# Performance work log

Measured on AMD Instinct MI355X. Metric: run time of the kernel, lower is better.

## Reference

```python
import jax, jax.numpy as jnp
import numpy as np

N = 100000       # num nodes
E = 1600000      # num edges (before self loops)
IN = 128         # in_channels
H = 4            # heads (layer 1)
C = 64           # hidden_channels
BN_EPS = 1e-5
NEG_SLOPE = 0.2  # PyG GATConv default


def setup_inputs() -> dict:
    key = jax.random.key(0)
    ks = jax.random.split(key, 12)
    s = lambda k, shape: jax.random.normal(k, shape, jnp.float32) * 0.05
    return {
        "x": jax.random.normal(ks[0], (N, IN), jnp.float32),
        "edge_index": jax.random.randint(ks[1], (2, E), 0, N),
        # GATConv layer 1: in=128 -> 64 per head, 4 heads, concat
        "W1": s(ks[2], (IN, H * C)),
        "a_src1": s(ks[3], (H, C)),
        "a_dst1": s(ks[4], (H, C)),
        "b1": jnp.zeros((H * C,), jnp.float32),
        # BatchNorm1d(256), eval mode with default running stats
        "bn_gamma": jnp.ones((H * C,), jnp.float32),
        "bn_beta": jnp.zeros((H * C,), jnp.float32),
        # GATConv layer 2: 256 -> 1, heads=1, concat=False
        "W2": s(ks[5], (H * C, 1)),
        "a_src2": s(ks[6], (1, 1)),
        "a_dst2": s(ks[7], (1, 1)),
        "b2": jnp.zeros((1,), jnp.float32),
        # risk predictor MLP: Linear(1,64) -> ReLU -> Linear(64,1) -> Sigmoid
        "mlp_w1": s(ks[8], (1, C)),
        "mlp_b1": jnp.zeros((C,), jnp.float32),
        "mlp_w2": s(ks[9], (C, 1)),
        "mlp_b2": jnp.zeros((1,), jnp.float32),
    }


def gat_conv(x, W, a_s, a_d, b, src, dst, n, concat):
    """PyG-style GATConv (self loops already appended to src/dst)."""
    h_, c_ = a_s.shape
    h = (x @ W).reshape(n, h_, c_)                       # [N,H,C]
    alpha_src = jnp.einsum('nhc,hc->nh', h, a_s)          # [N,H]
    alpha_dst = jnp.einsum('nhc,hc->nh', h, a_d)          # [N,H]
    alpha = jax.nn.leaky_relu(alpha_src[src] + alpha_dst[dst], NEG_SLOPE)  # [E,H]
    # segment softmax over destination nodes (self loops guarantee nonempty segments)
    amax = jax.ops.segment_max(alpha, dst, num_segments=n)
    ex = jnp.exp(alpha - amax[dst])
    den = jax.ops.segment_sum(ex, dst, num_segments=n)
    coef = ex / den[dst]                                  # [E,H]
    out = jax.ops.segment_sum(h[src] * coef[..., None], dst, num_segments=n)  # [N,H,C]
    out = out.reshape(n, h_ * c_) if concat else out.mean(axis=1)
    return out + b


def reference(x, edge_index, W1, a_src1, a_dst1, b1, bn_gamma, bn_beta,
              W2, a_src2, a_dst2, b2, mlp_w1, mlp_b1, mlp_w2, mlp_b2):
    n = x.shape[0]
    loops = jnp.arange(n)
    src = jnp.concatenate([edge_index[0], loops])
    dst = jnp.concatenate([edge_index[1], loops])

    h = gat_conv(x, W1, a_src1, a_dst1, b1, src, dst, n, concat=True)   # [N,256]
    # BatchNorm1d eval: running_mean=0, running_var=1
    h = h / jnp.sqrt(jnp.float32(1.0 + BN_EPS)) * bn_gamma + bn_beta
    h = jax.nn.elu(h)
    # dropout is identity in eval mode
    h = gat_conv(h, W2, a_src2, a_dst2, b2, src, dst, n, concat=False)  # [N,1]

    risk = jax.nn.relu(h @ mlp_w1 + mlp_b1)
    risk = jax.nn.sigmoid(risk @ mlp_w2 + mlp_b2)                        # [N,1]
    return risk
```

## Files before the change

kernel.cpp:

```cpp
#include <hip/hip_runtime.h>
#include <math.h>

#define NSL 0.2f
#define BSH 8
#define CAP 4608
#define ECHUNK 4096
#define MAXNB 512

typedef __attribute__((ext_vector_type(8))) short bf16x8;
typedef __attribute__((ext_vector_type(4))) float f32x4;
typedef __attribute__((ext_vector_type(2))) float floatx2;

__device__ __forceinline__ unsigned short f2b(float f){
  unsigned int u = __builtin_bit_cast(unsigned int, f);
  u = (u + 0x7FFFu + ((u >> 16) & 1u)) >> 16;
  return (unsigned short)u;
}
__device__ __forceinline__ unsigned cvtpk_bf16(float a, float b){
  unsigned r; asm("v_cvt_pk_bf16_f32 %0, %1, %2" : "=v"(r) : "v"(a), "v"(b)); return r;
}
__device__ __forceinline__ void pkfma(floatx2& a, floatx2 x, floatx2 w){
  asm("v_pk_fma_f32 %0, %1, %2, %0" : "+v"(a) : "v"(x), "v"(w));
}

__global__ __launch_bounds__(256) void k_fused1(const float* __restrict__ W, unsigned short* __restrict__ wt,
                                                const int* __restrict__ esrc, const int* __restrict__ edst,
                                                int E, int NB, int* gCur, unsigned* __restrict__ ebuf,
                                                int prepBlocks){
  __shared__ int hist[MAXNB];
  __shared__ int base[MAXNB];
  int bid = blockIdx.x, t = threadIdx.x;
  if (bid < prepBlocks){
    int idx = bid*256 + t;
    int k = idx >> 8, ch = idx & 255;
    wt[ch*128 + k] = f2b(W[idx]);
    return;
  }
  int b0 = bid - prepBlocks;
  for (int i=t;i<NB;i+=256) hist[i] = 0;
  __syncthreads();
  int e0 = b0*ECHUNK;
  int srcv[16], dstv[16];
  #pragma unroll
  for (int j=0;j<16;j++){
    int e = e0 + t + j*256;
    if (e < E){ srcv[j] = esrc[e]; dstv[j] = edst[e]; atomicAdd(&hist[dstv[j]>>BSH], 1); }
    else dstv[j] = -1;
  }
  __syncthreads();
  for (int i=t;i<NB;i+=256){
    int h = hist[i];
    base[i] = h > 0 ? atomicAdd(&gCur[i], h) : 0;
    hist[i] = 0;
  }
  __syncthreads();
  #pragma unroll
  for (int j=0;j<16;j++){
    if (dstv[j] >= 0){
      int b = dstv[j]>>BSH;
      int pos = base[b] + atomicAdd(&hist[b], 1);
      if (pos < CAP)
        ebuf[(size_t)b*CAP + pos] = (unsigned)srcv[j] | ((unsigned)(dstv[j] & 255) << 17);
    }
  }
}

__global__ __launch_bounds__(256) void k_fused2(const unsigned short* __restrict__ w1t,
                                                const float* __restrict__ x,
                                                const float* __restrict__ a_s1,
                                                const float* __restrict__ a_d1,
                                                unsigned char* __restrict__ h1f8,
                                                float* __restrict__ asrc, float* __restrict__ adst,
                                                int N, int gemmBlocks,
                                                const int* __restrict__ gCur, const unsigned* __restrict__ ebuf,
                                                int* __restrict__ rows, int* __restrict__ deg,
                                                int* __restrict__ csr){
  __shared__ union SM {
    unsigned short xs[64][132];
    struct { int lcnt[256]; int rofs[256]; int csr_l[CAP+256]; } c;
  } sm;
  int tid = threadIdx.x;
  int bid = blockIdx.x;

  if (bid < gemmBlocks){
    int lane = tid & 63, w = tid >> 6;
    int g = lane >> 4, nr = lane & 15;
    int n0 = bid*64;
    #pragma unroll
    for (int i=0;i<8;i++){
      int idx = tid + i*256;
      int node = idx >> 5, c4 = idx & 31;
      int gn = n0 + node;
      float4 v = (gn < N) ? *(const float4*)&x[(size_t)gn*128 + c4*4] : make_float4(0,0,0,0);
      uint2 pk = { cvtpk_bf16(v.x, v.y), cvtpk_bf16(v.z, v.w) };
      *(uint2*)&sm.xs[node][c4*4] = pk;
    }
    __syncthreads();

    int node_f[4]; bool val_f[4];
    #pragma unroll
    for (int fn=0;fn<4;fn++){ node_f[fn] = n0 + fn*16 + nr; val_f[fn] = node_f[fn] < N; }

    f32x4 acc[4][4] = {};
    #pragma unroll
    for (int s=0;s<4;s++){
      int ks = s*32;
      bf16x8 af[4], bf[4];
      #pragma unroll
      for (int fm=0;fm<4;fm++){
        int ch = w*64 + fm*16 + nr;
        const ushort4 lo = *(const ushort4*)(w1t + ch*128 + ks + 4*g);
        const ushort4 hi = *(const ushort4*)(w1t + ch*128 + ks + 16 + 4*g);
        af[fm] = (bf16x8){ (short)lo.x,(short)lo.y,(short)lo.z,(short)lo.w,
                           (short)hi.x,(short)hi.y,(short)hi.z,(short)hi.w };
      }
      #pragma unroll
      for (int fn=0;fn<4;fn++){
        union { uint2 u2[2]; bf16x8 v; } bb;
        bb.u2[0] = *(const uint2*)&sm.xs[fn*16 + nr][ks + 4*g];
        bb.u2[1] = *(const uint2*)&sm.xs[fn*16 + nr][ks + 16 + 4*g];
        bf[fn] = bb.v;
      }
      #pragma unroll
      for (int fm=0;fm<4;fm++)
        #pragma unroll
        for (int fn=0;fn<4;fn++)
          acc[fm][fn] = __builtin_amdgcn_mfma_f32_16x16x32_bf16(af[fm], bf[fn], acc[fm][fn], 0, 0, 0);
    }

    float ps[4] = {0.f,0.f,0.f,0.f}, pd[4] = {0.f,0.f,0.f,0.f};
    #pragma unroll
    for (int fm=0;fm<4;fm++){
      int cb = w*64 + fm*16 + g*4;
      float4 av = *(const float4*)&a_s1[cb];
      float4 dv = *(const float4*)&a_d1[cb];
      #pragma unroll
      for (int fn=0;fn<4;fn++){
        f32x4 c = acc[fm][fn];
        if (val_f[fn]){
          int u = __builtin_amdgcn_cvt_pk_fp8_f32(c[0], c[1], 0, false);
          u = __builtin_amdgcn_cvt_pk_fp8_f32(c[2], c[3], u, true);
          *(unsigned int*)(h1f8 + (size_t)node_f[fn]*256 + cb) = (unsigned int)u;
        }
        ps[fn] += c[0]*av.x + c[1]*av.y + c[2]*av.z + c[3]*av.w;
        pd[fn] += c[0]*dv.x + c[1]*dv.y + c[2]*dv.z + c[3]*dv.w;
      }
    }
    #pragma unroll
    for (int fn=0;fn<4;fn++){
      ps[fn] += __shfl_xor(ps[fn], 16); ps[fn] += __shfl_xor(ps[fn], 32);
      pd[fn] += __shfl_xor(pd[fn], 16); pd[fn] += __shfl_xor(pd[fn], 32);
      if (g == 0 && val_f[fn]){
        asrc[node_f[fn]*4 + w] = ps[fn];
        adst[node_f[fn]*4 + w] = pd[fn];
      }
    }
  } else {
    int b = bid - gemmBlocks;
    int node0 = b<<BSH;
    int nNodes = min(256, N - node0);
    int cnt_b = min(gCur[b], CAP);
    sm.c.lcnt[tid] = 0;
    __syncthreads();
    const unsigned* eb = ebuf + (size_t)b*CAP;
    for (int i=tid;i<cnt_b;i+=256) atomicAdd(&sm.c.lcnt[eb[i]>>17], 1);
    __syncthreads();
    int v = (tid < nNodes) ? (sm.c.lcnt[tid] + 1) : 0;
    sm.c.rofs[tid] = v; __syncthreads();
    #pragma unroll
    for (int o=1;o<256;o<<=1){
      int xv = (tid>=o) ? sm.c.rofs[tid-o] : 0; __syncthreads();
      sm.c.rofs[tid] += xv; __syncthreads();
    }
    int excl = sm.c.rofs[tid] - v;
    if (tid < nNodes) sm.c.csr_l[excl] = node0 + tid;
    sm.c.lcnt[tid] = excl + 1;
    __syncthreads();
    for (int i=tid;i<cnt_b;i+=256){
      unsigned e = eb[i];
      int pos = atomicAdd(&sm.c.lcnt[e>>17], 1);
      sm.c.csr_l[pos] = (int)(e & 0x1FFFFu);
    }
    __syncthreads();
    int total = sm.c.rofs[255];
    int gbase = b*(CAP+256);
    for (int i=tid;i<total;i+=256) csr[gbase+i] = sm.c.csr_l[i];
    if (tid < nNodes){ rows[node0+tid] = gbase + excl; deg[node0+tid] = v; }
  }
}

__global__ __launch_bounds__(256) void k_agg1(const int* __restrict__ rows, const int* __restrict__ deg,
                                              const int* __restrict__ csr,
                                              const unsigned char* __restrict__ h1f8,
                                              const float* __restrict__ asrc, const float* __restrict__ adst,
                                              const float* __restrict__ b1,
                                              const float* __restrict__ gamma, const float* __restrict__ beta,
                                              const float* __restrict__ W2,
                                              float* __restrict__ h2, int N){
  int lane = threadIdx.x & 63, wv = threadIdx.x >> 6;
  int node = blockIdx.x*4 + wv;
  if (node >= N) return;
  int slot = lane >> 4, l4 = lane & 15;
  int head = l4 >> 2;
  int rs = rows[node], d = deg[node];
  float adh = adst[node*4 + head];
  const uint4* h1u4 = (const uint4*)h1f8;
  floatx2 acc2[8];
  #pragma unroll
  for (int j=0;j<8;j++){ acc2[j][0] = 0.f; acc2[j][1] = 0.f; }
  float den = 0.f;
  int i = slot;
  if (i < d){
    int s = csr[rs+i];
    float aa = asrc[s*4 + head];
    uint4 v = h1u4[(size_t)s*16 + l4];
    while (true){
      int in = i + 4;
      bool hn = in < d;
      int sn = hn ? csr[rs+in] : 0;
      float al = aa + adh;
      al = fmaxf(al, NSL*al);
      float wgt = __expf(al);
      den += wgt;
      floatx2 ww; ww[0] = wgt; ww[1] = wgt;
      floatx2 f;
      f = __builtin_amdgcn_cvt_pk_f32_fp8(v.x, false); pkfma(acc2[0], f, ww);
      f = __builtin_amdgcn_cvt_pk_f32_fp8(v.x, true ); pkfma(acc2[1], f, ww);
      f = __builtin_amdgcn_cvt_pk_f32_fp8(v.y, false); pkfma(acc2[2], f, ww);
      f = __builtin_amdgcn_cvt_pk_f32_fp8(v.y, true ); pkfma(acc2[3], f, ww);
      f = __builtin_amdgcn_cvt_pk_f32_fp8(v.z, false); pkfma(acc2[4], f, ww);
      f = __builtin_amdgcn_cvt_pk_f32_fp8(v.z, true ); pkfma(acc2[5], f, ww);
      f = __builtin_amdgcn_cvt_pk_f32_fp8(v.w, false); pkfma(acc2[6], f, ww);
      f = __builtin_amdgcn_cvt_pk_f32_fp8(v.w, true ); pkfma(acc2[7], f, ww);
      if (!hn) break;
      i = in;
      aa = asrc[sn*4 + head];
      v = h1u4[(size_t)sn*16 + l4];
    }
  }
  #pragma unroll
  for (int j=0;j<8;j++){
    acc2[j][0] += __shfl_xor(acc2[j][0],16); acc2[j][1] += __shfl_xor(acc2[j][1],16);
    acc2[j][0] += __shfl_xor(acc2[j][0],32); acc2[j][1] += __shfl_xor(acc2[j][1],32);
  }
  den += __shfl_xor(den,16); den += __shfl_xor(den,32);
  float inv = 1.f/den;
  const float bsc = 0.99999500003749968f;
  int c = l4*16;
  float p = 0.f;
  #pragma unroll
  for (int q=0;q<4;q++){
    int cq = c + q*4;
    float4 bb = *(const float4*)&b1[cq];
    float4 gg = *(const float4*)&gamma[cq];
    float4 be = *(const float4*)&beta[cq];
    float4 w2_ = *(const float4*)&W2[cq];
    float o0 = (acc2[q*2+0][0]*inv + bb.x)*bsc*gg.x + be.x;
    float o1 = (acc2[q*2+0][1]*inv + bb.y)*bsc*gg.y + be.y;
    float o2 = (acc2[q*2+1][0]*inv + bb.z)*bsc*gg.z + be.z;
    float o3 = (acc2[q*2+1][1]*inv + bb.w)*bsc*gg.w + be.w;
    o0 = (o0>0.f)?o0:(__expf(o0)-1.f); o1 = (o1>0.f)?o1:(__expf(o1)-1.f);
    o2 = (o2>0.f)?o2:(__expf(o2)-1.f); o3 = (o3>0.f)?o3:(__expf(o3)-1.f);
    p += o0*w2_.x + o1*w2_.y + o2*w2_.z + o3*w2_.w;
  }
  p += __shfl_xor(p,1); p += __shfl_xor(p,2); p += __shfl_xor(p,4); p += __shfl_xor(p,8);
  if (lane == 0) h2[node] = p;
}

__global__ __launch_bounds__(256) void k_agg2(const int* __restrict__ rows, const int* __restrict__ deg,
                       const int* __restrict__ csr, const float* __restrict__ h2,
                       const float* __restrict__ as2, const float* __restrict__ ad2,
                       const float* __restrict__ b2,
                       const float* __restrict__ mw1, const float* __restrict__ mb1,
                       const float* __restrict__ mw2, const float* __restrict__ mb2,
                       float* __restrict__ out, int N){
  int t = threadIdx.x;
  int g16 = t >> 4, l = t & 15;
  int n = blockIdx.x*16 + g16;
  if (n >= N) return;
  float a_s = as2[0], a_d = ad2[0];
  float hd = h2[n];
  float ad = hd * a_d;
  int rs = rows[n], d = deg[n];
  float den = 0.f, num = 0.f;
  for (int i=l;i<d;i+=16){
    int s = csr[rs+i];
    float hs = h2[s];
    float al = hs*a_s + ad;
    al = fmaxf(al, NSL*al);
    float w = __expf(al);
    den += w; num += w*hs;
  }
  #pragma unroll
  for (int o=1;o<16;o<<=1){ den += __shfl_xor(den,o); num += __shfl_xor(num,o); }
  float o2 = num/den + b2[0];
  float acc = 0.f;
  #pragma unroll
  for (int q=0;q<4;q++){
    int j = l + q*16;
    float r = fmaxf(o2*mw1[j] + mb1[j], 0.f);
    acc += r*mw2[j];
  }
  #pragma unroll
  for (int o=1;o<16;o<<=1) acc += __shfl_xor(acc,o);
  if (l == 0) out[n] = 1.f/(1.f + __expf(-(acc + mb2[0])));
}

extern "C" void kernel_launch(void* const* d_in, const int* in_sizes, int n_in,
                              void* d_out, int out_size, void* d_ws, size_t ws_size,
                              hipStream_t stream){
  const float* x   = (const float*)d_in[0];
  const int*   ei  = (const int*)  d_in[1];
  const float* W1  = (const float*)d_in[2];
  const float* as1 = (const float*)d_in[3];
  const float* ad1 = (const float*)d_in[4];
  const float* b1  = (const float*)d_in[5];
  const float* gam = (const float*)d_in[6];
  const float* bet = (const float*)d_in[7];
  const float* W2  = (const float*)d_in[8];
  const float* as2 = (const float*)d_in[9];
  const float* ad2 = (const float*)d_in[10];
  const float* b2  = (const float*)d_in[11];
  const float* mw1 = (const float*)d_in[12];
  const float* mb1 = (const float*)d_in[13];
  const float* mw2 = (const float*)d_in[14];
  const float* mb2 = (const float*)d_in[15];
  float* out = (float*)d_out;

  int N = in_sizes[0] / 128;
  int E = in_sizes[1] / 2;
  const int* esrc = ei;
  const int* edst = ei + E;
  int NB = (N + 255) >> 8;

  char* p = (char*)d_ws;
  auto alloc = [&](size_t bytes)->char*{ char* r = p; p += (bytes + 255) & ~(size_t)255; return r; };
  int*      deg   = (int*)     alloc((size_t)N*4);
  int*      rows  = (int*)     alloc((size_t)N*4);
  int*      gCur  = (int*)     alloc((size_t)NB*4);
  unsigned* ebuf  = (unsigned*)alloc((size_t)NB*CAP*4);
  int*      csr   = (int*)     alloc((size_t)NB*(CAP+256)*4);
  unsigned short* w1t  = (unsigned short*)alloc((size_t)256*128*2);
  unsigned char*  h1f8 = (unsigned char*) alloc((size_t)N*256);
  float* asrc  = (float*)alloc((size_t)N*4*4);
  float* adst  = (float*)alloc((size_t)N*4*4);
  float* h2    = (float*)alloc((size_t)N*4);

  hipMemsetAsync(gCur, 0, (size_t)NB*4, stream);

  int prepBlocks = 128;
  int nbA = (E + ECHUNK - 1)/ECHUNK;
  k_fused1<<<prepBlocks + nbA, 256, 0, stream>>>(W1, w1t, esrc, edst, E, NB, gCur, ebuf, prepBlocks);

  int gemmBlocks = (N + 63)/64;
  k_fused2<<<gemmBlocks + NB, 256, 0, stream>>>(w1t, x, as1, ad1, h1f8, asrc, adst,
                                                N, gemmBlocks, gCur, ebuf, rows, deg, csr);

  k_agg1<<<(N+3)/4,256,0,stream>>>(rows, deg, csr, h1f8, asrc, adst, b1, gam, bet, W2, h2, N);

  k_agg2<<<(N+15)/16,256,0,stream>>>(rows, deg, csr, h2, as2, ad2, b2, mw1, mb1, mw2, mb2, out, N);
}
```

Baseline: 217.3 us.

## Quantize layer-1 features to FP4 with per-node-per-head scales

```diff
diff --git a/kernel.cpp b/kernel.cpp
--- a/kernel.cpp
+++ b/kernel.cpp
@@ -6,6 +6,21 @@
 #define CAP 4608
 #define ECHUNK 4096
 #define MAXNB 512
+
+#if defined(__has_builtin)
+#if __has_builtin(__builtin_amdgcn_cvt_scalef32_pk_f32_fp4) && __has_builtin(__builtin_amdgcn_cvt_scalef32_pk_fp4_f32)
+#define HAS_FP4 1
+#endif
+#endif
+#ifndef HAS_FP4
+#define HAS_FP4 0
+#endif
+
+#if HAS_FP4
+#define ROWB 128
+#else
+#define ROWB 256
+#endif
 
 typedef __attribute__((ext_vector_type(8))) short bf16x8;
 typedef __attribute__((ext_vector_type(4))) float f32x4;
@@ -69,8 +84,8 @@
                                                 const float* __restrict__ x,
                                                 const float* __restrict__ a_s1,
                                                 const float* __restrict__ a_d1,
-                                                unsigned char* __restrict__ h1f8,
-                                                float* __restrict__ asrc, float* __restrict__ adst,
+                                                unsigned char* __restrict__ h1q,
+                                                float2* __restrict__ asz, float* __restrict__ adst,
                                                 int N, int gemmBlocks,
                                                 const int* __restrict__ gCur, const unsigned* __restrict__ ebuf,
                                                 int* __restrict__ rows, int* __restrict__ deg,
@@ -128,7 +143,7 @@
           acc[fm][fn] = __builtin_amdgcn_mfma_f32_16x16x32_bf16(af[fm], bf[fn], acc[fm][fn], 0, 0, 0);
     }
 
-    float ps[4] = {0.f,0.f,0.f,0.f}, pd[4] = {0.f,0.f,0.f,0.f};
+    float ps[4] = {0.f,0.f,0.f,0.f}, pd[4] = {0.f,0.f,0.f,0.f}, qm[4] = {0.f,0.f,0.f,0.f};
     #pragma unroll
     for (int fm=0;fm<4;fm++){
       int cb = w*64 + fm*16 + g*4;
@@ -137,21 +152,51 @@
       #pragma unroll
       for (int fn=0;fn<4;fn++){
         f32x4 c = acc[fm][fn];
-        if (val_f[fn]){
-          int u = __builtin_amdgcn_cvt_pk_fp8_f32(c[0], c[1], 0, false);
-          u = __builtin_amdgcn_cvt_pk_fp8_f32(c[2], c[3], u, true);
-          *(unsigned int*)(h1f8 + (size_t)node_f[fn]*256 + cb) = (unsigned int)u;
-        }
         ps[fn] += c[0]*av.x + c[1]*av.y + c[2]*av.z + c[3]*av.w;
         pd[fn] += c[0]*dv.x + c[1]*dv.y + c[2]*dv.z + c[3]*dv.w;
+        qm[fn] = fmaxf(qm[fn], fmaxf(fmaxf(fabsf(c[0]),fabsf(c[1])), fmaxf(fabsf(c[2]),fabsf(c[3]))));
       }
     }
     #pragma unroll
     for (int fn=0;fn<4;fn++){
       ps[fn] += __shfl_xor(ps[fn], 16); ps[fn] += __shfl_xor(ps[fn], 32);
       pd[fn] += __shfl_xor(pd[fn], 16); pd[fn] += __shfl_xor(pd[fn], 32);
+      qm[fn] = fmaxf(qm[fn], __shfl_xor(qm[fn], 16));
+      qm[fn] = fmaxf(qm[fn], __shfl_xor(qm[fn], 32));
+    }
+    #pragma unroll
+    for (int fn=0;fn<4;fn++){
+      if (!val_f[fn]) continue;
+#if HAS_FP4
+      float inv = 6.f / fmaxf(qm[fn], 1e-20f);
+      #pragma unroll
+      for (int fm=0;fm<4;fm++){
+        int cb = w*64 + fm*16 + g*4;
+        f32x4 c = acc[fm][fn];
+        unsigned d0 = __builtin_amdgcn_cvt_scalef32_pk_fp4_f32(0u, c[0]*inv, c[1]*inv, 1.0f, 0);
+        d0 = __builtin_amdgcn_cvt_scalef32_pk_fp4_f32(d0, c[2]*inv, c[3]*inv, 1.0f, 1);
+        *(unsigned short*)(h1q + (size_t)node_f[fn]*ROWB + (cb>>1)) = (unsigned short)(d0 & 0xFFFFu);
+      }
+#else
+      #pragma unroll
+      for (int fm=0;fm<4;fm++){
+        int cb = w*64 + fm*16 + g*4;
+        f32x4 c = acc[fm][fn];
+        int u = __builtin_amdgcn_cvt_pk_fp8_f32(c[0], c[1], 0, false);
+        u = __builtin_amdgcn_cvt_pk_fp8_f32(c[2], c[3], u, true);
+        *(unsigned int*)(h1q + (size_t)node_f[fn]*ROWB + cb) = (unsigned int)u;
+      }
+#endif
+    }
+    #pragma unroll
+    for (int fn=0;fn<4;fn++){
       if (g == 0 && val_f[fn]){
-        asrc[node_f[fn]*4 + w] = ps[fn];
+#if HAS_FP4
+        float scl = qm[fn] * (1.f/6.f);
+#else
+        float scl = 1.f;
+#endif
+        asz[node_f[fn]*4 + w] = make_float2(ps[fn], scl);
         adst[node_f[fn]*4 + w] = pd[fn];
       }
     }
@@ -191,8 +236,8 @@
 
 __global__ __launch_bounds__(256) void k_agg1(const int* __restrict__ rows, const int* __restrict__ deg,
                                               const int* __restrict__ csr,
-                                              const unsigned char* __restrict__ h1f8,
-                                              const float* __restrict__ asrc, const float* __restrict__ adst,
+                                              const unsigned char* __restrict__ h1q,
+                                              const float2* __restrict__ asz, const float* __restrict__ adst,
                                               const float* __restrict__ b1,
                                               const float* __restrict__ gamma, const float* __restrict__ beta,
                                               const float* __restrict__ W2,
@@ -204,26 +249,41 @@
   int head = l4 >> 2;
   int rs = rows[node], d = deg[node];
   float adh = adst[node*4 + head];
-  const uint4* h1u4 = (const uint4*)h1f8;
   floatx2 acc2[8];
   #pragma unroll
   for (int j=0;j<8;j++){ acc2[j][0] = 0.f; acc2[j][1] = 0.f; }
   float den = 0.f;
+#if HAS_FP4
+  const uint2* h1v = (const uint2*)h1q;
+#else
+  const uint4* h1v = (const uint4*)h1q;
+#endif
   int i = slot;
   if (i < d){
     int s = csr[rs+i];
-    float aa = asrc[s*4 + head];
-    uint4 v = h1u4[(size_t)s*16 + l4];
+    float2 t = asz[s*4 + head];
+    auto v = h1v[(size_t)s*16 + l4];
     while (true){
       int in = i + 4;
       bool hn = in < d;
       int sn = hn ? csr[rs+in] : 0;
-      float al = aa + adh;
+      float al = t.x + adh;
       al = fmaxf(al, NSL*al);
       float wgt = __expf(al);
       den += wgt;
-      floatx2 ww; ww[0] = wgt; ww[1] = wgt;
+      float wq = wgt * t.y;
+      floatx2 ww; ww[0] = wq; ww[1] = wq;
       floatx2 f;
+#if HAS_FP4
+      f = __builtin_bit_cast(floatx2, __builtin_amdgcn_cvt_scalef32_pk_f32_fp4(v.x, 1.0f, 0)); pkfma(acc2[0], f, ww);
+      f = __builtin_bit_cast(floatx2, __builtin_amdgcn_cvt_scalef32_pk_f32_fp4(v.x, 1.0f, 1)); pkfma(acc2[1], f, ww);
+      f = __builtin_bit_cast(floatx2, __builtin_amdgcn_cvt_scalef32_pk_f32_fp4(v.x, 1.0f, 2)); pkfma(acc2[2], f, ww);
+      f = __builtin_bit_cast(floatx2, __builtin_amdgcn_cvt_scalef32_pk_f32_fp4(v.x, 1.0f, 3)); pkfma(acc2[3], f, ww);
+      f = __builtin_bit_cast(floatx2, __builtin_amdgcn_cvt_scalef32_pk_f32_fp4(v.y, 1.0f, 0)); pkfma(acc2[4], f, ww);
+      f = __builtin_bit_cast(floatx2, __builtin_amdgcn_cvt_scalef32_pk_f32_fp4(v.y, 1.0f, 1)); pkfma(acc2[5], f, ww);
+      f = __builtin_bit_cast(floatx2, __builtin_amdgcn_cvt_scalef32_pk_f32_fp4(v.y, 1.0f, 2)); pkfma(acc2[6], f, ww);
+      f = __builtin_bit_cast(floatx2, __builtin_amdgcn_cvt_scalef32_pk_f32_fp4(v.y, 1.0f, 3)); pkfma(acc2[7], f, ww);
+#else
       f = __builtin_amdgcn_cvt_pk_f32_fp8(v.x, false); pkfma(acc2[0], f, ww);
       f = __builtin_amdgcn_cvt_pk_f32_fp8(v.x, true ); pkfma(acc2[1], f, ww);
       f = __builtin_amdgcn_cvt_pk_f32_fp8(v.y, false); pkfma(acc2[2], f, ww);
@@ -232,10 +292,11 @@
       f = __builtin_amdgcn_cvt_pk_f32_fp8(v.z, true ); pkfma(acc2[5], f, ww);
       f = __builtin_amdgcn_cvt_pk_f32_fp8(v.w, false); pkfma(acc2[6], f, ww);
       f = __builtin_amdgcn_cvt_pk_f32_fp8(v.w, true ); pkfma(acc2[7], f, ww);
+#endif
       if (!hn) break;
       i = in;
-      aa = asrc[sn*4 + head];
-      v = h1u4[(size_t)sn*16 + l4];
+      t = asz[sn*4 + head];
+      v = h1v[(size_t)sn*16 + l4];
     }
   }
   #pragma unroll
@@ -341,10 +402,10 @@
   unsigned* ebuf  = (unsigned*)alloc((size_t)NB*CAP*4);
   int*      csr   = (int*)     alloc((size_t)NB*(CAP+256)*4);
   unsigned short* w1t  = (unsigned short*)alloc((size_t)256*128*2);
-  unsigned char*  h1f8 = (unsigned char*) alloc((size_t)N*256);
-  float* asrc  = (float*)alloc((size_t)N*4*4);
-  float* adst  = (float*)alloc((size_t)N*4*4);
-  float* h2    = (float*)alloc((size_t)N*4);
+  unsigned char*  h1q  = (unsigned char*) alloc((size_t)N*ROWB);
+  float2*   asz   = (float2*)  alloc((size_t)N*4*8);
+  float*    adst  = (float*)   alloc((size_t)N*4*4);
+  float*    h2    = (float*)   alloc((size_t)N*4);
 
   hipMemsetAsync(gCur, 0, (size_t)NB*4, stream);
 
@@ -353,10 +414,10 @@
   k_fused1<<<prepBlocks + nbA, 256, 0, stream>>>(W1, w1t, esrc, edst, E, NB, gCur, ebuf, prepBlocks);
 
   int gemmBlocks = (N + 63)/64;
-  k_fused2<<<gemmBlocks + NB, 256, 0, stream>>>(w1t, x, as1, ad1, h1f8, asrc, adst,
+  k_fused2<<<gemmBlocks + NB, 256, 0, stream>>>(w1t, x, as1, ad1, h1q, asz, adst,
                                                 N, gemmBlocks, gCur, ebuf, rows, deg, csr);
 
-  k_agg1<<<(N+3)/4,256,0,stream>>>(rows, deg, csr, h1f8, asrc, adst, b1, gam, bet, W2, h2, N);
+  k_agg1<<<(N+3)/4,256,0,stream>>>(rows, deg, csr, h1q, asz, adst, b1, gam, bet, W2, h2, N);
 
   k_agg2<<<(N+15)/16,256,0,stream>>>(rows, deg, csr, h2, as2, ad2, b2, mw1, mb1, mw2, mb2, out, N);
 }
```

Measured after the change: 224.4 us. 3.3% more time.
